# Performance work log

Hardware: AMD Instinct MI355X
Metric: run time of the kernel (lower is better)

The kernel has to match this reference:

```python
import jax, jax.numpy as jnp
import numpy as np

B, T, IN, H, OUT = 64, 32, 256, 512, 256
M, W, R = 256, 64, 4            # nr_cells, cell_size, read_heads
NN_IN = IN + R * W              # 512
NN_OUT = H + R * W              # 768
IFACE = R * W + 3 * W + 5 * R + 3  # 471
CLIP = 20.0
DELTA = 1e-6


def setup_inputs():
    key = jax.random.key(0)
    ks = jax.random.split(key, 10)
    s = 0.05
    bound = float(np.sqrt(6.0 / (B * H + 2 * H)))  # xavier_uniform on (2,B,H)
    return {
        'x': jax.random.normal(ks[0], (B, T, IN), jnp.float32),
        'h0': jax.random.uniform(ks[1], (2, B, H), jnp.float32, -bound, bound),
        'Wih0': jax.random.normal(ks[2], (4 * H, NN_IN), jnp.float32) * s,
        'Whh0': jax.random.normal(ks[3], (4 * H, H), jnp.float32) * s,
        'bih0': jnp.zeros((4 * H,), jnp.float32),
        'bhh0': jnp.zeros((4 * H,), jnp.float32),
        'Wih1': jax.random.normal(ks[4], (4 * H, H), jnp.float32) * s,
        'Whh1': jax.random.normal(ks[5], (4 * H, H), jnp.float32) * s,
        'bih1': jnp.zeros((4 * H,), jnp.float32),
        'bhh1': jnp.zeros((4 * H,), jnp.float32),
        'Wif': jax.random.normal(ks[6], (IFACE, H), jnp.float32) * s,
        'bif': jnp.zeros((IFACE,), jnp.float32),
        'Wout': jax.random.normal(ks[7], (OUT, NN_OUT), jnp.float32) * s,
        'bout': jnp.zeros((OUT,), jnp.float32),
    }


def _lstm_cell(x, h, c, Wih, Whh, bih, bhh):
    g = x @ Wih.T + bih + h @ Whh.T + bhh
    i, f, gg, o = jnp.split(g, 4, axis=1)  # torch gate order i,f,g,o
    c = jax.nn.sigmoid(f) * c + jax.nn.sigmoid(i) * jnp.tanh(gg)
    h = jax.nn.sigmoid(o) * jnp.tanh(c)
    return h, c


def _content_weights(mem, keys, strengths):
    # mem: (b,M,W), keys: (b,K,W), strengths: (b,K) -> softmax over M
    mem_n = mem / (jnp.linalg.norm(mem, axis=2, keepdims=True) + DELTA)
    key_n = keys / (jnp.linalg.norm(keys, axis=2, keepdims=True) + DELTA)
    sim = jnp.einsum('bkw,bmw->bkm', key_n, mem_n)
    return jax.nn.softmax(sim * strengths[..., None], axis=2)


def _memory_step(xi, mem, link, prec, rw, ww, usage):
    b = xi.shape[0]
    o = 0
    rk = jnp.tanh(xi[:, :R * W].reshape(b, R, W)); o = R * W
    rs = jax.nn.softplus(xi[:, o:o + R]); o += R
    wk = jnp.tanh(xi[:, o:o + W]).reshape(b, 1, W); o += W
    ws = jax.nn.softplus(xi[:, o])[:, None]; o += 1
    ev = jax.nn.sigmoid(xi[:, o:o + W]); o += W
    wv = jnp.tanh(xi[:, o:o + W]); o += W
    fg = jax.nn.sigmoid(xi[:, o:o + R]); o += R
    ag = jax.nn.sigmoid(xi[:, o])[:, None]; o += 1
    wg = jax.nn.sigmoid(xi[:, o])[:, None]; o += 1
    rm = jax.nn.softmax(xi[:, o:o + 3 * R].reshape(b, R, 3), axis=2)

    # usage update (uses OLD read/write weights); single write head
    usage = usage + (1.0 - usage) * ww
    psi = jnp.prod(1.0 - fg[:, :, None] * rw, axis=1)
    usage = usage * psi

    # write content addressing on OLD memory
    wcw = _content_weights(mem, wk, ws)[:, 0]  # (b,M)

    # allocation by ascending sort of usage (exclusive cumprod)
    u = DELTA + (1.0 - DELTA) * usage
    phi = jnp.argsort(u, axis=1)
    sorted_u = jnp.take_along_axis(u, phi, axis=1)
    excl = jnp.cumprod(jnp.concatenate([jnp.ones((b, 1), u.dtype), sorted_u], axis=1), axis=1)[:, :-1]
    sorted_alloc = (1.0 - sorted_u) * excl
    alloc = jnp.take_along_axis(sorted_alloc, jnp.argsort(phi, axis=1), axis=1)

    ww = wg * (ag * alloc + (1.0 - ag) * wcw)  # (b,M)

    # erase + write
    mem = mem * (1.0 - ww[:, :, None] * ev[:, None, :]) + ww[:, :, None] * wv[:, None, :]

    # temporal link matrix + precedence
    prev_scale = 1.0 - ww[:, :, None] - ww[:, None, :]
    link = prev_scale * link + ww[:, :, None] * prec[:, None, :]
    link = link * (1.0 - jnp.eye(M, dtype=link.dtype))
    prec = (1.0 - ww.sum(axis=1, keepdims=True)) * prec + ww

    # read: directional weights use NEW link and OLD read weights; content uses NEW memory
    rcw = _content_weights(mem, rk, rs)               # (b,R,M)
    fwd = jnp.einsum('bij,brj->bri', link, rw)
    bwd = jnp.einsum('brj,bji->bri', rw, link)
    rw = rm[:, :, 0:1] * bwd + rm[:, :, 1:2] * fwd + rm[:, :, 2:3] * rcw
    rvec = jnp.einsum('brm,bmw->brw', rw, mem).reshape(b, R * W)
    return rvec, mem, link, prec, rw, ww, usage


def reference(x, h0, Wih0, Whh0, bih0, bhh0, Wih1, Whh1, bih1, bhh1, Wif, bif, Wout, bout):
    b = x.shape[0]
    lr0 = jnp.zeros((b, R * W), x.dtype)  # initial last_read; NOTE: source concatenates this
    # initial zero last_read to EVERY timestep's controller input (inputs built upfront)
    carry0 = (h0[0], h0[0], h0[1], h0[1],
              jnp.full((b, M, W), DELTA, x.dtype),   # memory
              jnp.zeros((b, M, M), x.dtype),          # link matrix
              jnp.zeros((b, M), x.dtype),             # precedence
              jnp.full((b, R, M), DELTA, x.dtype),    # read weights
              jnp.full((b, M), DELTA, x.dtype),       # write weights
              jnp.zeros((b, M), x.dtype))             # usage

    def step(carry, x_t):
        h0_, c0_, h1_, c1_, mem, link, prec, rw, ww, usage = carry
        inp = jnp.concatenate([x_t, lr0], axis=1)
        h0_, c0_ = _lstm_cell(inp, h0_, c0_, Wih0, Whh0, bih0, bhh0)
        h1_, c1_ = _lstm_cell(h0_, h1_, c1_, Wih1, Whh1, bih1, bhh1)
        out = jnp.clip(h1_, -CLIP, CLIP)
        xi = out @ Wif.T + bif
        rvec, mem, link, prec, rw, ww, usage = _memory_step(xi, mem, link, prec, rw, ww, usage)
        o_t = jnp.concatenate([out, rvec], axis=1)  # (b, NN_OUT)
        return (h0_, c0_, h1_, c1_, mem, link, prec, rw, ww, usage), o_t

    _, ys = jax.lax.scan(step, carry0, jnp.swapaxes(x, 0, 1))  # (T,b,NN_OUT)
    outputs = jnp.tanh(ys) @ Wout.T + bout  # Dropout(p=0) -> Tanh -> Linear
    return jnp.swapaxes(outputs, 0, 1)      # (b,T,OUT)
```

## Files before the change

kernel.cpp:

```cpp
#include <hip/hip_runtime.h>
#include <hip/hip_bf16.h>
#include <math.h>


typedef __bf16 bf16_t;
typedef __attribute__((ext_vector_type(8))) __bf16 bf16x8;
typedef __attribute__((ext_vector_type(4))) float f32x4;

#define B_    64
#define T_    32
#define IN_   256
#define H_    512
#define M_    256
#define W_    64
#define R_    4
#define IFACE_ 471
#define DELTA_ 1e-6f

#define OFF_H0SEQ  (0L)
#define SZ_H0SEQ   (32L*64*512*2)
#define OFF_OUTSEQ (OFF_H0SEQ + SZ_H0SEQ)
#define SZ_OUTSEQ  (32L*64*512*2)
#define OFF_H0BUF  (OFF_OUTSEQ + SZ_OUTSEQ)
#define SZ_HBUF    (2L*64*512*2)
#define OFF_H1BUF  (OFF_H0BUF + SZ_HBUF)
#define OFF_XI     (OFF_H1BUF + SZ_HBUF)
#define SZ_XI      (32L*64*480*4)
#define OFF_RVEC   (OFF_XI + SZ_XI)
#define SZ_RVEC    (32L*64*256*4)
#define OFF_YBF    (OFF_RVEC + SZ_RVEC)
#define SZ_YBF     (32L*64*768*2)
#define OFF_BAR    (OFF_YBF + SZ_YBF)
#define SZ_BAR     (256L)
#define OFF_XB     (OFF_BAR + SZ_BAR)
#define SZ_XB      (64L*32*256*2)
#define OFF_H0B    (OFF_XB + SZ_XB)
#define SZ_H0B     (2L*64*512*2)
#define OFF_W0     (OFF_H0B + SZ_H0B)
#define SZ_W       (2048L*512*2)
#define OFF_W1     (OFF_W0 + SZ_W)
#define OFF_W2     (OFF_W1 + SZ_W)
#define OFF_W3     (OFF_W2 + SZ_W)
#define OFF_WIF    (OFF_W3 + SZ_W)
#define SZ_WIF     (480L*512*2)
#define OFF_WOUTB  (OFF_WIF + SZ_WIF)
#define SZ_WOUTB   (256L*768*2)
#define OFF_BS0    (OFF_WOUTB + SZ_WOUTB)
#define SZ_BS      (2048L*4)
#define OFF_BS1    (OFF_BS0 + SZ_BS)
#define OFF_BIF    (OFF_BS1 + SZ_BS)
#define SZ_BIF     (2048L)
#define OFF_BOUTF  (OFF_BIF + SZ_BIF)
#define SZ_BOUTF   (1024L)
#define OFF_FLG    (OFF_BOUTF + SZ_BOUTF)
#define SZ_FLG     (4096L)

__device__ __forceinline__ float frcp(float x){ return __builtin_amdgcn_rcpf(x); }
__device__ __forceinline__ float fsqrt_(float x){ return __builtin_amdgcn_sqrtf(x); }
__device__ __forceinline__ float sigf(float x){ return frcp(1.0f + __expf(-x)); }
__device__ __forceinline__ float tanh_f(float x){
  float xc = fminf(fmaxf(x, -44.0f), 44.0f);
  float t = __expf(2.0f * xc);
  return (t - 1.0f) * frcp(t + 1.0f);
}
__device__ __forceinline__ float softplusf(float x){
  return fmaxf(x, 0.0f) + __logf(1.0f + __expf(-fabsf(x)));
}
__device__ __forceinline__ float wred(float v){
  #pragma unroll
  for (int off = 32; off; off >>= 1) v += __shfl_xor(v, off, 64);
  return v;
}
__device__ __forceinline__ float ldin(const void* p, long i, int mf){
  return mf ? ((const float*)p)[i] : (float)((const bf16_t*)p)[i];
}

__device__ __forceinline__ unsigned flag_ld(const unsigned* p){
  return __hip_atomic_load(p, __ATOMIC_RELAXED, __HIP_MEMORY_SCOPE_AGENT);
}

__device__ __forceinline__ void flagbar(unsigned* flg, int bid, unsigned tgt,
                                        int tid, int lane, int wv){
  __syncthreads();
  if (tid == 0)
    __hip_atomic_store(flg + (size_t)bid*16, tgt, __ATOMIC_RELEASE,
                       __HIP_MEMORY_SCOPE_AGENT);
  if (wv == 0){
    for (;;){
      unsigned f = flag_ld(flg + (size_t)lane*16);
      if (__all(f >= tgt)) break;
      __builtin_amdgcn_s_sleep(2);
    }
    __builtin_amdgcn_fence(__ATOMIC_ACQUIRE, "agent");
  }
  __syncthreads();
}

__global__ void k_detect(const unsigned short* __restrict__ x16,
                         int* __restrict__ flag, unsigned* __restrict__ bar,
                         unsigned* __restrict__ flg){
  __shared__ int cnt;
  if (threadIdx.x == 0){ cnt = 0; bar[0] = 0u; bar[1] = 0u; }
  for (int i = threadIdx.x; i < 1024; i += 256) flg[i] = 0u;
  __syncthreads();
  unsigned short u = x16[threadIdx.x * 2];
  int e = (u >> 7) & 0xFF;
  if (e >= 0x88) atomicAdd(&cnt, 1);
  __syncthreads();
  if (threadIdx.x == 0) *flag = (cnt > 16) ? 1 : 0;
}

__global__ void k_convert(const void* x, const void* h0, const void* Wih0,
                          const void* Whh0, const void* bih0, const void* bhh0,
                          const void* Wih1, const void* Whh1, const void* bih1,
                          const void* bhh1, const void* Wif, const void* bif,
                          const void* Wout, const void* bout,
                          bf16_t* __restrict__ xb, bf16_t* __restrict__ h0b,
                          bf16_t* __restrict__ h0buf, bf16_t* __restrict__ h1buf,
                          bf16_t* __restrict__ W0, bf16_t* __restrict__ W1,
                          bf16_t* __restrict__ W2, bf16_t* __restrict__ W3,
                          bf16_t* __restrict__ Wifp, bf16_t* __restrict__ Woutb,
                          float* __restrict__ bs0, float* __restrict__ bs1,
                          float* __restrict__ bifp, float* __restrict__ boutf,
                          const int* __restrict__ flag)
{
  const int mf = *flag;
  const long stride = (long)gridDim.x * blockDim.x;
  long i0 = (long)blockIdx.x * blockDim.x + threadIdx.x;
  switch (blockIdx.y){
  case 0: for (long i = i0; i < 64L*32*256; i += stride) xb[i] = (bf16_t)ldin(x, i, mf); break;
  case 1: for (long i = i0; i < 2L*64*512; i += stride){
            float v = ldin(h0, i, mf); bf16_t bb = (bf16_t)v; h0b[i] = bb;
            if (i < 64*512) h0buf[i] = bb; else h1buf[i - 64*512] = bb;
          } break;
  case 2: for (long i = i0; i < 2048L*512; i += stride) W0[i] = (bf16_t)ldin(Wih0, i, mf); break;
  case 3: for (long i = i0; i < 2048L*512; i += stride) W1[i] = (bf16_t)ldin(Whh0, i, mf); break;
  case 4: for (long i = i0; i < 2048L*512; i += stride) W2[i] = (bf16_t)ldin(Wih1, i, mf); break;
  case 5: for (long i = i0; i < 2048L*512; i += stride) W3[i] = (bf16_t)ldin(Whh1, i, mf); break;
  case 6: for (long i = i0; i < 480L*512; i += stride){
            long r = i >> 9;
            Wifp[i] = (r < IFACE_) ? (bf16_t)ldin(Wif, i, mf) : (bf16_t)0.0f;
          } break;
  case 7: for (long i = i0; i < 256L*768; i += stride) Woutb[i] = (bf16_t)ldin(Wout, i, mf); break;
  case 8:
    for (long i = i0; i < 2048; i += stride){
      bs0[i] = ldin(bih0, i, mf) + ldin(bhh0, i, mf);
      bs1[i] = ldin(bih1, i, mf) + ldin(bhh1, i, mf);
    }
    for (long i = i0; i < 480; i += stride) bifp[i] = (i < IFACE_) ? ldin(bif, i, mf) : 0.0f;
    for (long i = i0; i < 256; i += stride) boutf[i] = ldin(bout, i, mf);
    break;
  }
}

__device__ __forceinline__ void softmax256_wave(float* a, int lane){
  float v0=a[lane], v1=a[64+lane], v2=a[128+lane], v3=a[192+lane];
  float mx = fmaxf(fmaxf(v0,v1), fmaxf(v2,v3));
  #pragma unroll
  for (int off=32; off; off>>=1) mx = fmaxf(mx, __shfl_xor(mx, off, 64));
  v0=__expf(v0-mx); v1=__expf(v1-mx); v2=__expf(v2-mx); v3=__expf(v3-mx);
  float s = v0+v1+v2+v3;
  #pragma unroll
  for (int off=32; off; off>>=1) s += __shfl_xor(s, off, 64);
  float inv = frcp(s);
  a[lane]=v0*inv; a[64+lane]=v1*inv; a[128+lane]=v2*inv; a[192+lane]=v3*inv;
}

struct ProdShm {
  bf16_t wpool[66560];
  float  cst[64][16];
  float  bias[4][16];
};
struct ConsShm {
  float smem[256][65];
  float rkn4r[2][65][4];
  float wkn[64], ev_[64], wvv[64];
  float rs_[4], fg_[4], rm_[4][3];
  float wsS, agS, wgS, wwsumS;
  float invn[256], wcw[256];
  float usage[256], uu[256], su[256], scanA[256];
  int   rank_[256];
  float ww_[256], prec_[256];
  float rw_[4][256];
  float rw4[256][4];
  float fwd_[4][256], bwd_[4][256], rcw_[4][256];
  bf16_t rwb[4][264];
  float p2cT[2][264];
  float p5cT[5][2][264];
};
union ShUnion { ProdShm p; ConsShm c; };

__global__ __launch_bounds__(512) void k_main(
    const bf16_t* __restrict__ xb, const bf16_t* __restrict__ h0b,
    const bf16_t* __restrict__ W0, const bf16_t* __restrict__ W1,
    const bf16_t* __restrict__ W2, const bf16_t* __restrict__ W3,
    const float* __restrict__ bs0, const float* __restrict__ bs1,
    const bf16_t* __restrict__ Wifp, const float* __restrict__ bifp,
    bf16_t* __restrict__ h0buf, bf16_t* __restrict__ h1buf,
    bf16_t* __restrict__ h0seq, bf16_t* __restrict__ outseq,
    float* __restrict__ XI, float* __restrict__ RVEC,
    unsigned* __restrict__ flg)
{
  __shared__ ShUnion sh;
  const int bid = blockIdx.x;
  const int tid = threadIdx.x, lane = tid & 63, wv = tid >> 6;
  const int m16 = lane & 15, q = lane >> 4;

  if (bid < 64){
    ProdShm& P = sh.p;
    const int layer = bid >> 5;
    const int u0 = (bid & 31) * 16;

    if (!layer){
      for (int i = tid; i < 64*32; i += 512){
        int rl = i >> 5, c8 = (i & 31)*8;
        int grow = (rl >> 4)*512 + u0 + (rl & 15);
        *(bf16x8*)&P.wpool[rl*264 + c8] = *(const bf16x8*)(W0 + (size_t)grow*512 + c8);
      }
      for (int i = tid; i < 64*64; i += 512){
        int rl = i >> 6, c8 = (i & 63)*8;
        int grow = (rl >> 4)*512 + u0 + (rl & 15);
        *(bf16x8*)&P.wpool[16896 + rl*520 + c8] = *(const bf16x8*)(W1 + (size_t)grow*512 + c8);
      }
    } else {
      for (int i = tid; i < 64*64; i += 512){
        int rl = i >> 6, c8 = (i & 63)*8;
        int grow = (rl >> 4)*512 + u0 + (rl & 15);
        *(bf16x8*)&P.wpool[rl*520 + c8]         = *(const bf16x8*)(W2 + (size_t)grow*512 + c8);
        *(bf16x8*)&P.wpool[33280 + rl*520 + c8] = *(const bf16x8*)(W3 + (size_t)grow*512 + c8);
      }
    }
    for (int i = tid; i < 64*16; i += 512){
      int b = i >> 4, n = i & 15;
      P.cst[b][n] = (float)h0b[layer*(64*512) + b*512 + u0 + n];
    }
    if (tid < 64){
      int G = tid >> 4, n = tid & 15;
      const float* bs = layer ? bs1 : bs0;
      P.bias[G][n] = bs[G*512 + u0 + n];
    }
    __syncthreads();

    bf16_t* hbuf = layer ? h1buf : h0buf;

    for (int ps = 0; ps <= 33; ++ps){
      if (wv < 4){
        const int t = layer ? (ps - 1) : ps;
        const bool active = layer ? (ps >= 1 && ps <= 32) : (ps < 32);
        if (active){
          const int p = t & 1;
          const bf16_t* hin = hbuf + p*(64*512);
          bf16_t* hout = hbuf + (p^1)*(64*512);
          const int b0 = wv * 16;

          f32x4 acc[4];
          #pragma unroll
          for (int G = 0; G < 4; ++G){ float bv = P.bias[G][m16]; acc[G] = (f32x4){bv,bv,bv,bv}; }

          if (!layer){
            #pragma unroll 2
            for (int kt = 0; kt < 8; ++kt){
              bf16x8 a = *(const bf16x8*)(xb + ((size_t)(b0+m16)*T_ + t)*IN_ + kt*32 + q*8);
              #pragma unroll
              for (int G = 0; G < 4; ++G)
                acc[G] = __builtin_amdgcn_mfma_f32_16x16x32_bf16(
                    a, *(const bf16x8*)&P.wpool[(G*16+m16)*264 + kt*32 + q*8], acc[G], 0, 0, 0);
            }
            #pragma unroll 4
            for (int kt = 0; kt < 16; ++kt){
              bf16x8 a = *(const bf16x8*)(hin + (b0+m16)*512 + kt*32 + q*8);
              #pragma unroll
              for (int G = 0; G < 4; ++G)
                acc[G] = __builtin_amdgcn_mfma_f32_16x16x32_bf16(
                    a, *(const bf16x8*)&P.wpool[16896 + (G*16+m16)*520 + kt*32 + q*8], acc[G], 0, 0, 0);
            }
          } else {
            #pragma unroll 4
            for (int kt = 0; kt < 16; ++kt){
              bf16x8 a = *(const bf16x8*)(h0seq + ((size_t)t*64 + b0+m16)*512 + kt*32 + q*8);
              #pragma unroll
              for (int G = 0; G < 4; ++G)
                acc[G] = __builtin_amdgcn_mfma_f32_16x16x32_bf16(
                    a, *(const bf16x8*)&P.wpool[(G*16+m16)*520 + kt*32 + q*8], acc[G], 0, 0, 0);
            }
            #pragma unroll 4
            for (int kt = 0; kt < 16; ++kt){
              bf16x8 a = *(const bf16x8*)(hin + (b0+m16)*512 + kt*32 + q*8);
              #pragma unroll
              for (int G = 0; G < 4; ++G)
                acc[G] = __builtin_amdgcn_mfma_f32_16x16x32_bf16(
                    a, *(const bf16x8*)&P.wpool[33280 + (G*16+m16)*520 + kt*32 + q*8], acc[G], 0, 0, 0);
            }
          }
          #pragma unroll
          for (int v = 0; v < 4; ++v){
            int b = b0 + q*4 + v;
            float gi = acc[0][v], gf = acc[1][v], gg = acc[2][v], go = acc[3][v];
            float c_ = sigf(gf)*P.cst[b][m16] + sigf(gi)*tanh_f(gg);
            P.cst[b][m16] = c_;
            float h = sigf(go)*tanh_f(c_);
            bf16_t hb = (bf16_t)h;
            hout[b*512 + u0 + m16] = hb;
            if (!layer) h0seq[((size_t)t*64 + b)*512 + u0 + m16] = hb;
            else        outseq[((size_t)t*64 + b)*512 + u0 + m16] = hb;
          }
        }
      } else if (ps >= 2 && bid < 30){
        const int t2 = ps - 2;
        const int b0 = (wv - 4) * 16;
        const int r = bid*16 + m16;
        float bv = bifp[r];
        f32x4 acc = {bv,bv,bv,bv};
        const bf16_t* arow = outseq + ((size_t)t2*64 + b0 + m16)*512 + q*8;
        const bf16_t* brow = Wifp + (size_t)r*512 + q*8;
        #pragma unroll 4
        for (int kt = 0; kt < 16; ++kt){
          acc = __builtin_amdgcn_mfma_f32_16x16x32_bf16(
              *(const bf16x8*)(arow + kt*32), *(const bf16x8*)(brow + kt*32), acc, 0, 0, 0);
        }
        #pragma unroll
        for (int v = 0; v < 4; ++v)
          XI[((size_t)t2*64 + b0 + q*4 + v)*480 + r] = acc[v];
      }
      flagbar(flg, bid, (unsigned)(ps + 1), tid, lane, wv);
    }
  } else {
    ConsShm& S = sh.c;
    const int b = bid - 64;
    const int quad = lane >> 4, li = lane & 15;

    bf16x8 rowL[2][8], colL[2][8];
    #pragma unroll
    for (int g = 0; g < 2; ++g)
      #pragma unroll
      for (int ch = 0; ch < 8; ++ch)
        #pragma unroll
        for (int z = 0; z < 8; ++z){ rowL[g][ch][z] = (bf16_t)0.0f; colL[g][ch][z] = (bf16_t)0.0f; }

    float mr[32];
    #pragma unroll
    for (int z = 0; z < 32; ++z) mr[z] = DELTA_;

    int off0 = -1, off1 = -1, off2 = -1;
    if (wv < 4)            off0 = wv*64 + lane;
    else if (wv == 4)      off0 = 260 + lane;
    else if (wv == 5)      off0 = 325 + lane;
    else if (wv == 6)      off0 = 389 + lane;
    else {
      if (lane < 4)        off0 = 256 + lane;
      else if (lane == 4)  off0 = 324;
      else if (lane < 9)   off0 = 453 + (lane - 5);
      else if (lane == 9)  off0 = 457;
      else if (lane == 10) off0 = 458;
      else if (lane >= 16 && lane < 20){
        off0 = 459 + (lane - 16)*3; off1 = off0 + 1; off2 = off0 + 2;
      }
    }

    if (tid < 256){
      S.ww_[tid] = DELTA_; S.usage[tid] = 0.0f; S.prec_[tid] = 0.0f;
      S.invn[tid] = 1.0f/(fsqrt_(64.0f*DELTA_*DELTA_) + DELTA_);
      #pragma unroll
      for (int r = 0; r < 4; ++r) S.rw_[r][tid] = DELTA_;
    }
    for (int i = tid; i < 4*264; i += 512) ((bf16_t*)S.rwb)[i] = (bf16_t)DELTA_;
    for (int i = tid; i < 256*65; i += 512) ((float*)S.smem)[i] = DELTA_;
    __syncthreads();

    const int mH = tid >> 1, q2 = tid & 1;

    if (wv == 0){
      for (;;){
        unsigned f = flag_ld(flg + (size_t)lane*16);
        if (__all(f >= 3u)) break;
        __builtin_amdgcn_s_sleep(2);
      }
      __builtin_amdgcn_fence(__ATOMIC_ACQUIRE, "agent");
    }
    __syncthreads();
    float x0 = 0.0f, x1 = 0.0f, x2 = 0.0f;
    {
      const float* xp = XI + (size_t)b*480;
      if (off0 >= 0) x0 = xp[off0];
      if (off1 >= 0){ x1 = xp[off1]; x2 = xp[off2]; }
    }

    for (int t = 0; t < 32; ++t){
      if (wv < 4){
        float v = tanh_f(x0);
        float s = wred(v*v);
        float vn = v * frcp(fsqrt_(s) + DELTA_);
        S.rkn4r[0][lane][wv] = vn; S.rkn4r[1][lane][wv] = vn;
      } else if (wv == 4){
        float v = tanh_f(x0);
        float s = wred(v*v);
        S.wkn[lane] = v * frcp(fsqrt_(s) + DELTA_);
      } else if (wv == 5){ S.ev_[lane] = sigf(x0);
      } else if (wv == 6){ S.wvv[lane] = tanh_f(x0);
      } else {
        if (lane < 4)        S.rs_[lane] = softplusf(x0);
        else if (lane == 4)  S.wsS = softplusf(x0);
        else if (lane < 9)   S.fg_[lane-5] = sigf(x0);
        else if (lane == 9)  S.agS = sigf(x0);
        else if (lane == 10) S.wgS = sigf(x0);
        else if (lane >= 16 && lane < 20){
          int r = lane - 16;
          float mx = fmaxf(x0, fmaxf(x1, x2));
          float e0 = __expf(x0-mx), e1 = __expf(x1-mx), e2 = __expf(x2-mx);
          float inv = frcp(e0+e1+e2);
          S.rm_[r][0]=e0*inv; S.rm_[r][1]=e1*inv; S.rm_[r][2]=e2*inv;
        }
      }
      __syncthreads();

      if (tid < 256){
        int m = tid;
        float us = S.usage[m] + (1.0f - S.usage[m])*S.ww_[m];
        float psi = (1.0f - S.fg_[0]*S.rw_[0][m]) * (1.0f - S.fg_[1]*S.rw_[1][m])
                  * (1.0f - S.fg_[2]*S.rw_[2][m]) * (1.0f - S.fg_[3]*S.rw_[3][m]);
        us *= psi;
        S.usage[m] = us;
        S.uu[m] = DELTA_ + (1.0f - DELTA_)*us;
      }
      { float acc = 0.0f;
        #pragma unroll
        for (int it = 0; it < 32; ++it){
          int w = q2*32 + it;
          acc += mr[it] * S.wkn[w];
        }
        S.p2cT[q2][mH] = acc; }
      __syncthreads();

      if (wv == 0){
        #pragma unroll
        for (int z = 0; z < 4; ++z){
          int m = z*64 + lane;
          S.wcw[m] = S.wsS * (S.p2cT[0][m] + S.p2cT[1][m]) * S.invn[m];
        }
        softmax256_wave(S.wcw, lane);
      } else if (tid >= 256){
        const int i = tid - 256;
        const float ui = S.uu[i];
        int cnt = 0;
        #pragma unroll 8
        for (int k = 0; k < 64; ++k){
          f32x4 u4 = *(const f32x4*)&S.uu[k*4];
          #pragma unroll
          for (int z = 0; z < 4; ++z){
            int j = k*4 + z; float uj = u4[z];
            cnt += (uj < ui || (uj == ui && j < i)) ? 1 : 0;
          }
        }
        S.rank_[i] = cnt;
        S.su[cnt] = ui;
      }
      __syncthreads();

      if (wv == 0){
        int base = lane*4;
        float v0 = S.su[base], v1 = S.su[base+1], v2 = S.su[base+2];
        float p1 = v0*v1, p2 = p1*v2, p3 = p2*S.su[base+3];
        float sc = p3;
        #pragma unroll
        for (int off = 1; off < 64; off <<= 1){
          float n = __shfl_up(sc, off, 64);
          if (lane >= off) sc *= n;
        }
        float exch = __shfl_up(sc, 1, 64);
        if (lane == 0) exch = 1.0f;
        S.scanA[base] = exch; S.scanA[base+1] = exch*v0;
        S.scanA[base+2] = exch*p1; S.scanA[base+3] = exch*p2;
      }
      __syncthreads();

      { const int m = mH;
        float al = (1.0f - S.uu[m]) * S.scanA[S.rank_[m]];
        float wm = S.wgS*(S.agS*al + (1.0f - S.agS)*S.wcw[m]);
        if (q2 == 0) S.ww_[m] = wm;
        float s2 = 0.0f, sr0 = 0.0f, sr1 = 0.0f, sr2 = 0.0f, sr3 = 0.0f;
        #pragma unroll
        for (int it = 0; it < 32; ++it){
          int w = q2*32 + it;
          float mn = mr[it]*(1.0f - wm*S.ev_[w]) + wm*S.wvv[w];
          mr[it] = mn;
          S.smem[m][w] = mn;
          s2 += mn*mn;
          f32x4 rk = *(const f32x4*)&S.rkn4r[q2][w][0];
          sr0 += mn*rk[0]; sr1 += mn*rk[1]; sr2 += mn*rk[2]; sr3 += mn*rk[3];
        }
        S.p5cT[0][q2][m] = s2;
        S.p5cT[1][q2][m] = sr0; S.p5cT[2][q2][m] = sr1;
        S.p5cT[3][q2][m] = sr2; S.p5cT[4][q2][m] = sr3; }
      __syncthreads();

      if (tid < 256){
        int m = tid;
        float s2 = S.p5cT[0][0][m] + S.p5cT[0][1][m];
        float inv = frcp(fsqrt_(s2) + DELTA_);
        S.invn[m] = inv;
        #pragma unroll
        for (int r = 0; r < 4; ++r){
          float sr = S.p5cT[r+1][0][m] + S.p5cT[r+1][1][m];
          S.rcw_[r][m] = S.rs_[r]*sr*inv;
        }
      } else if (wv == 4){
        float s = wred(S.ww_[lane] + S.ww_[64+lane] + S.ww_[128+lane] + S.ww_[192+lane]);
        if (lane == 0) S.wwsumS = s;
      }
      { float wown[2], pown[2], alpha[2];
        #pragma unroll
        for (int g = 0; g < 2; ++g){
          int o = wv*32 + g*16 + li;
          wown[g] = S.ww_[o]; pown[g] = S.prec_[o];
          alpha[g] = 1.0f - wown[g];
        }
        f32x4 facc[2] = {{0,0,0,0},{0,0,0,0}}, bacc[2] = {{0,0,0,0},{0,0,0,0}};
        #pragma unroll
        for (int ch = 0; ch < 8; ++ch){
          const int cbase = ch*32 + quad*8;
          bf16x8 rwf = *(const bf16x8*)&S.rwb[li & 3][cbase];
          f32x4 wA = *(const f32x4*)&S.ww_[cbase];
          f32x4 wB = *(const f32x4*)&S.ww_[cbase+4];
          f32x4 pA = *(const f32x4*)&S.prec_[cbase];
          f32x4 pB = *(const f32x4*)&S.prec_[cbase+4];
          float wcf[8] = {wA[0],wA[1],wA[2],wA[3],wB[0],wB[1],wB[2],wB[3]};
          float pcf[8] = {pA[0],pA[1],pA[2],pA[3],pB[0],pB[1],pB[2],pB[3]};
          #pragma unroll
          for (int g = 0; g < 2; ++g){
            const int o = wv*32 + g*16 + li;
            bf16x8 rl = rowL[g][ch];
            bf16x8 cl = colL[g][ch];
            #pragma unroll
            for (int jj = 0; jj < 8; ++jj){
              const int c = cbase + jj;
              float s = alpha[g] - wcf[jj];
              float vr = s*(float)rl[jj] + wown[g]*pcf[jj];
              float vc = s*(float)cl[jj] + wcf[jj]*pown[g];
              if (c == o){ vr = 0.0f; vc = 0.0f; }
              rl[jj] = (bf16_t)vr;
              cl[jj] = (bf16_t)vc;
            }
            rowL[g][ch] = rl; colL[g][ch] = cl;
            facc[g] = __builtin_amdgcn_mfma_f32_16x16x32_bf16(rl, rwf, facc[g], 0, 0, 0);
            bacc[g] = __builtin_amdgcn_mfma_f32_16x16x32_bf16(rwf, cl, bacc[g], 0, 0, 0);
          }
        }
        #pragma unroll
        for (int g = 0; g < 2; ++g){
          if (li < 4){
            #pragma unroll
            for (int z = 0; z < 4; ++z) S.fwd_[li][wv*32 + g*16 + quad*4 + z] = facc[g][z];
          }
          if (quad == 0){
            #pragma unroll
            for (int z = 0; z < 4; ++z) S.bwd_[z][wv*32 + g*16 + li] = bacc[g][z];
          }
        }
      }
      __syncthreads();

      if (wv < 4) softmax256_wave(S.rcw_[wv], lane);
      else {
        int m = tid - 256;
        float p = (1.0f - S.wwsumS)*S.prec_[m] + S.ww_[m];
        S.prec_[m] = p;
        if (wv == 4 && t < 31){
          const unsigned tgt = (unsigned)(t + 4);
          for (;;){
            unsigned f = flag_ld(flg + (size_t)lane*16);
            if (__all(f >= tgt)) break;
            __builtin_amdgcn_s_sleep(2);
          }
          __builtin_amdgcn_fence(__ATOMIC_ACQUIRE, "agent");
        }
      }
      __syncthreads();

      if (t < 31){
        const float* xp = XI + ((size_t)(t+1)*64 + b)*480;
        if (off0 >= 0) x0 = xp[off0];
        if (off1 >= 0){ x1 = xp[off1]; x2 = xp[off2]; }
      }
      { int r = tid >> 7, m0 = (tid & 127)*2;
        #pragma unroll
        for (int z = 0; z < 2; ++z){
          int m = m0 + z;
          float v = S.rm_[r][0]*S.bwd_[r][m] + S.rm_[r][1]*S.fwd_[r][m] + S.rm_[r][2]*S.rcw_[r][m];
          S.rw_[r][m] = v;
          S.rw4[m][r] = v;
          S.rwb[r][m] = (bf16_t)v;
        } }
      __syncthreads();

      { const int o = tid >> 1;
        const int r = o >> 6, w = o & 63;
        float s = 0.0f;
        #pragma unroll 16
        for (int k = 0; k < 128; ++k){
          int m = q2*128 + k;
          s += S.rw4[m][r] * S.smem[m][w];
        }
        s += __shfl_xor(s, 1, 64);
        if (q2 == 0) RVEC[((size_t)t*64 + b)*256 + o] = s;
      }
    }
  }
}

__global__ void k_tanhy(const bf16_t* __restrict__ outseq, const float* __restrict__ RVEC,
                        bf16_t* __restrict__ Y){
  const int n = 2048*768;
  for (int i = blockIdx.x*blockDim.x + threadIdx.x; i < n; i += gridDim.x*blockDim.x){
    int row = i / 768, j = i - row*768;
    float v = (j < 512) ? (float)outseq[(size_t)row*512 + j] : RVEC[(size_t)row*256 + (j - 512)];
    Y[i] = (bf16_t)tanh_f(v);
  }
}

__global__ __launch_bounds__(256,1) void k_out(
    const bf16_t* __restrict__ Y, const bf16_t* __restrict__ Woutb,
    const float* __restrict__ boutf, void* __restrict__ dout,
    const int* __restrict__ flag)
{
  const int mf = *flag;
  const int mt = blockIdx.x;
  const int tid = threadIdx.x, lane = tid & 63, wv = tid >> 6;
  const int nt = blockIdx.y*4 + wv;
  const int m16 = lane & 15, q = lane >> 4;
  const int o = nt*16 + m16;
  float bv = boutf[o];
  f32x4 acc = {bv,bv,bv,bv};
  const bf16_t* arow = Y + (size_t)(mt*16 + m16)*768 + q*8;
  const bf16_t* brow = Woutb + (size_t)o*768 + q*8;
  for (int kt = 0; kt < 24; ++kt){
    acc = __builtin_amdgcn_mfma_f32_16x16x32_bf16(
        *(const bf16x8*)(arow + kt*32), *(const bf16x8*)(brow + kt*32), acc, 0, 0, 0);
  }
  #pragma unroll
  for (int v = 0; v < 4; ++v){
    int row = mt*16 + q*4 + v;
    int b = row & 63, t = row >> 6;
    size_t idx = ((size_t)b*T_ + t)*256 + o;
    if (mf) ((float*)dout)[idx] = acc[v];
    else    ((bf16_t*)dout)[idx] = (bf16_t)acc[v];
  }
}

extern "C" void kernel_launch(void* const* d_in, const int* in_sizes, int n_in,
                              void* d_out, int out_size, void* d_ws, size_t ws_size,
                              hipStream_t stream)
{
  char* ws = (char*)d_ws;
  bf16_t* H0SEQ  = (bf16_t*)(ws + OFF_H0SEQ);
  bf16_t* OUTSEQ = (bf16_t*)(ws + OFF_OUTSEQ);
  bf16_t* H0BUF  = (bf16_t*)(ws + OFF_H0BUF);
  bf16_t* H1BUF  = (bf16_t*)(ws + OFF_H1BUF);
  float*  XI     = (float*) (ws + OFF_XI);
  float*  RVEC   = (float*) (ws + OFF_RVEC);
  bf16_t* YBF    = (bf16_t*)(ws + OFF_YBF);
  unsigned* BAR  = (unsigned*)(ws + OFF_BAR);
  int*    FLAG   = (int*)   (ws + OFF_BAR + 8);
  bf16_t* XB     = (bf16_t*)(ws + OFF_XB);
  bf16_t* H0B    = (bf16_t*)(ws + OFF_H0B);
  bf16_t* W0     = (bf16_t*)(ws + OFF_W0);
  bf16_t* W1     = (bf16_t*)(ws + OFF_W1);
  bf16_t* W2     = (bf16_t*)(ws + OFF_W2);
  bf16_t* W3     = (bf16_t*)(ws + OFF_W3);
  bf16_t* WIFP   = (bf16_t*)(ws + OFF_WIF);
  bf16_t* WOUTB  = (bf16_t*)(ws + OFF_WOUTB);
  float*  BS0    = (float*) (ws + OFF_BS0);
  float*  BS1    = (float*) (ws + OFF_BS1);
  float*  BIFP   = (float*) (ws + OFF_BIF);
  float*  BOUTF  = (float*) (ws + OFF_BOUTF);
  unsigned* FLG  = (unsigned*)(ws + OFF_FLG);

  k_detect<<<1, 256, 0, stream>>>((const unsigned short*)d_in[0], FLAG, BAR, FLG);
  k_convert<<<dim3(256, 9), 256, 0, stream>>>(
      d_in[0], d_in[1], d_in[2], d_in[3], d_in[4], d_in[5], d_in[6],
      d_in[7], d_in[8], d_in[9], d_in[10], d_in[11], d_in[12], d_in[13],
      XB, H0B, H0BUF, H1BUF, W0, W1, W2, W3, WIFP, WOUTB,
      BS0, BS1, BIFP, BOUTF, FLAG);
  k_main<<<128, 512, 0, stream>>>(XB, H0B, W0, W1, W2, W3, BS0, BS1,
                                  WIFP, BIFP, H0BUF, H1BUF, H0SEQ, OUTSEQ,
                                  XI, RVEC, FLG);
  k_tanhy<<<512, 256, 0, stream>>>(OUTSEQ, RVEC, YBF);
  k_out<<<dim3(128, 4), 256, 0, stream>>>(YBF, WOUTB, BOUTF, d_out, FLAG);
}
```

Before: 1.099 ms.

## Double block size to 1024 threads and repartition memory-step work across waves

Launches the persistent main kernel with 1024 threads per block. Consumer blocks split their per-row memory, link-matrix and read-vector work over 16 waves instead of 8: each thread holds fewer memory columns and link rows, the usage sort rank is computed in two halves and then combined, and the read-vector product becomes per-wave partial sums followed by a reduction. The aim is to shorten the serial per-timestep latency of the memory update by adding parallelism. In exchange it adds synchronisation barriers and shared-memory traffic, and the producer blocks' extra waves sit mostly idle while register pressure per thread is capped.

```diff
diff --git a/kernel.cpp b/kernel.cpp
--- a/kernel.cpp
+++ b/kernel.cpp
@@ -173,24 +173,26 @@
 };
 struct ConsShm {
   float smem[256][65];
-  float rkn4r[2][65][4];
+  float rkn4r[4][65][4];
   float wkn[64], ev_[64], wvv[64];
   float rs_[4], fg_[4], rm_[4][3];
   float wsS, agS, wgS, wwsumS;
   float invn[256], wcw[256];
   float usage[256], uu[256], su[256], scanA[256];
   int   rank_[256];
+  int   rankP[2][256];
   float ww_[256], prec_[256];
   float rw_[4][256];
   float rw4[256][4];
   float fwd_[4][256], bwd_[4][256], rcw_[4][256];
   bf16_t rwb[4][264];
-  float p2cT[2][264];
-  float p5cT[5][2][264];
+  float p4cT[4][264];
+  float p5cT[5][4][264];
+  float rvp[16][4][64];
 };
 union ShUnion { ProdShm p; ConsShm c; };
 
-__global__ __launch_bounds__(512) void k_main(
+__global__ __launch_bounds__(1024) void k_main(
     const bf16_t* __restrict__ xb, const bf16_t* __restrict__ h0b,
     const bf16_t* __restrict__ W0, const bf16_t* __restrict__ W1,
     const bf16_t* __restrict__ W2, const bf16_t* __restrict__ W3,
@@ -212,25 +214,25 @@
     const int u0 = (bid & 31) * 16;
 
     if (!layer){
-      for (int i = tid; i < 64*32; i += 512){
+      for (int i = tid; i < 64*32; i += 1024){
         int rl = i >> 5, c8 = (i & 31)*8;
         int grow = (rl >> 4)*512 + u0 + (rl & 15);
         *(bf16x8*)&P.wpool[rl*264 + c8] = *(const bf16x8*)(W0 + (size_t)grow*512 + c8);
       }
-      for (int i = tid; i < 64*64; i += 512){
+      for (int i = tid; i < 64*64; i += 1024){
         int rl = i >> 6, c8 = (i & 63)*8;
         int grow = (rl >> 4)*512 + u0 + (rl & 15);
         *(bf16x8*)&P.wpool[16896 + rl*520 + c8] = *(const bf16x8*)(W1 + (size_t)grow*512 + c8);
       }
     } else {
-      for (int i = tid; i < 64*64; i += 512){
+      for (int i = tid; i < 64*64; i += 1024){
         int rl = i >> 6, c8 = (i & 63)*8;
         int grow = (rl >> 4)*512 + u0 + (rl & 15);
         *(bf16x8*)&P.wpool[rl*520 + c8]         = *(const bf16x8*)(W2 + (size_t)grow*512 + c8);
         *(bf16x8*)&P.wpool[33280 + rl*520 + c8] = *(const bf16x8*)(W3 + (size_t)grow*512 + c8);
       }
     }
-    for (int i = tid; i < 64*16; i += 512){
+    for (int i = tid; i < 64*16; i += 1024){
       int b = i >> 4, n = i & 15;
       P.cst[b][n] = (float)h0b[layer*(64*512) + b*512 + u0 + n];
     }
@@ -305,7 +307,7 @@
             else        outseq[((size_t)t*64 + b)*512 + u0 + m16] = hb;
           }
         }
-      } else if (ps >= 2 && bid < 30){
+      } else if (wv < 8 && ps >= 2 && bid < 30){
         const int t2 = ps - 2;
         const int b0 = (wv - 4) * 16;
         const int r = bid*16 + m16;
@@ -329,24 +331,24 @@
     const int b = bid - 64;
     const int quad = lane >> 4, li = lane & 15;
 
-    bf16x8 rowL[2][8], colL[2][8];
+    const int orow = wv*16 + li;
+    bf16x8 rowL[8], colL[8];
     #pragma unroll
-    for (int g = 0; g < 2; ++g)
+    for (int ch = 0; ch < 8; ++ch)
       #pragma unroll
-      for (int ch = 0; ch < 8; ++ch)
-        #pragma unroll
-        for (int z = 0; z < 8; ++z){ rowL[g][ch][z] = (bf16_t)0.0f; colL[g][ch][z] = (bf16_t)0.0f; }
-
-    float mr[32];
+      for (int z = 0; z < 8; ++z){ rowL[ch][z] = (bf16_t)0.0f; colL[ch][z] = (bf16_t)0.0f; }
+
+    const int mQ = tid >> 2, q4 = tid & 3;
+    float mr[16];
     #pragma unroll
-    for (int z = 0; z < 32; ++z) mr[z] = DELTA_;
+    for (int z = 0; z < 16; ++z) mr[z] = DELTA_;
 
     int off0 = -1, off1 = -1, off2 = -1;
     if (wv < 4)            off0 = wv*64 + lane;
     else if (wv == 4)      off0 = 260 + lane;
     else if (wv == 5)      off0 = 325 + lane;
     else if (wv == 6)      off0 = 389 + lane;
-    else {
+    else if (wv == 7){
       if (lane < 4)        off0 = 256 + lane;
       else if (lane == 4)  off0 = 324;
       else if (lane < 9)   off0 = 453 + (lane - 5);
@@ -363,11 +365,9 @@
       #pragma unroll
       for (int r = 0; r < 4; ++r) S.rw_[r][tid] = DELTA_;
     }
-    for (int i = tid; i < 4*264; i += 512) ((bf16_t*)S.rwb)[i] = (bf16_t)DELTA_;
-    for (int i = tid; i < 256*65; i += 512) ((float*)S.smem)[i] = DELTA_;
+    for (int i = tid; i < 4*264; i += 1024) ((bf16_t*)S.rwb)[i] = (bf16_t)DELTA_;
+    for (int i = tid; i < 256*65; i += 1024) ((float*)S.smem)[i] = DELTA_;
     __syncthreads();
-
-    const int mH = tid >> 1, q2 = tid & 1;
 
     if (wv == 0){
       for (;;){
@@ -390,14 +390,15 @@
         float v = tanh_f(x0);
         float s = wred(v*v);
         float vn = v * frcp(fsqrt_(s) + DELTA_);
-        S.rkn4r[0][lane][wv] = vn; S.rkn4r[1][lane][wv] = vn;
+        #pragma unroll
+        for (int g = 0; g < 4; ++g) S.rkn4r[g][lane][wv] = vn;
       } else if (wv == 4){
         float v = tanh_f(x0);
         float s = wred(v*v);
         S.wkn[lane] = v * frcp(fsqrt_(s) + DELTA_);
       } else if (wv == 5){ S.ev_[lane] = sigf(x0);
       } else if (wv == 6){ S.wvv[lane] = tanh_f(x0);
-      } else {
+      } else if (wv == 7){
         if (lane < 4)        S.rs_[lane] = softplusf(x0);
         else if (lane == 4)  S.wsS = softplusf(x0);
         else if (lane < 9)   S.fg_[lane-5] = sigf(x0);
@@ -424,35 +425,42 @@
       }
       { float acc = 0.0f;
         #pragma unroll
-        for (int it = 0; it < 32; ++it){
-          int w = q2*32 + it;
+        for (int it = 0; it < 16; ++it){
+          int w = q4*16 + it;
           acc += mr[it] * S.wkn[w];
         }
-        S.p2cT[q2][mH] = acc; }
+        S.p4cT[q4][mQ] = acc; }
       __syncthreads();
 
       if (wv == 0){
         #pragma unroll
         for (int z = 0; z < 4; ++z){
           int m = z*64 + lane;
-          S.wcw[m] = S.wsS * (S.p2cT[0][m] + S.p2cT[1][m]) * S.invn[m];
+          S.wcw[m] = S.wsS * (S.p4cT[0][m] + S.p4cT[1][m] + S.p4cT[2][m] + S.p4cT[3][m]) * S.invn[m];
         }
         softmax256_wave(S.wcw, lane);
-      } else if (tid >= 256){
-        const int i = tid - 256;
+      } else if (tid >= 512){
+        const int idx = tid - 512;
+        const int i = idx & 255, half = idx >> 8;
         const float ui = S.uu[i];
         int cnt = 0;
         #pragma unroll 8
-        for (int k = 0; k < 64; ++k){
-          f32x4 u4 = *(const f32x4*)&S.uu[k*4];
+        for (int k = 0; k < 32; ++k){
+          f32x4 u4 = *(const f32x4*)&S.uu[half*128 + k*4];
           #pragma unroll
           for (int z = 0; z < 4; ++z){
-            int j = k*4 + z; float uj = u4[z];
+            int j = half*128 + k*4 + z; float uj = u4[z];
             cnt += (uj < ui || (uj == ui && j < i)) ? 1 : 0;
           }
         }
-        S.rank_[i] = cnt;
-        S.su[cnt] = ui;
+        S.rankP[half][i] = cnt;
+      }
+      __syncthreads();
+
+      if (tid < 256){
+        int rank = S.rankP[0][tid] + S.rankP[1][tid];
+        S.rank_[tid] = rank;
+        S.su[rank] = S.uu[tid];
       }
       __syncthreads();
 
@@ -473,48 +481,42 @@
       }
       __syncthreads();
 
-      { const int m = mH;
-        float al = (1.0f - S.uu[m]) * S.scanA[S.rank_[m]];
-        float wm = S.wgS*(S.agS*al + (1.0f - S.agS)*S.wcw[m]);
-        if (q2 == 0) S.ww_[m] = wm;
+      { float al = (1.0f - S.uu[mQ]) * S.scanA[S.rank_[mQ]];
+        float wm = S.wgS*(S.agS*al + (1.0f - S.agS)*S.wcw[mQ]);
+        if (q4 == 0) S.ww_[mQ] = wm;
         float s2 = 0.0f, sr0 = 0.0f, sr1 = 0.0f, sr2 = 0.0f, sr3 = 0.0f;
         #pragma unroll
-        for (int it = 0; it < 32; ++it){
-          int w = q2*32 + it;
+        for (int it = 0; it < 16; ++it){
+          int w = q4*16 + it;
           float mn = mr[it]*(1.0f - wm*S.ev_[w]) + wm*S.wvv[w];
           mr[it] = mn;
-          S.smem[m][w] = mn;
+          S.smem[mQ][w] = mn;
           s2 += mn*mn;
-          f32x4 rk = *(const f32x4*)&S.rkn4r[q2][w][0];
+          f32x4 rk = *(const f32x4*)&S.rkn4r[q4][w][0];
           sr0 += mn*rk[0]; sr1 += mn*rk[1]; sr2 += mn*rk[2]; sr3 += mn*rk[3];
         }
-        S.p5cT[0][q2][m] = s2;
-        S.p5cT[1][q2][m] = sr0; S.p5cT[2][q2][m] = sr1;
-        S.p5cT[3][q2][m] = sr2; S.p5cT[4][q2][m] = sr3; }
+        S.p5cT[0][q4][mQ] = s2;
+        S.p5cT[1][q4][mQ] = sr0; S.p5cT[2][q4][mQ] = sr1;
+        S.p5cT[3][q4][mQ] = sr2; S.p5cT[4][q4][mQ] = sr3; }
       __syncthreads();
 
       if (tid < 256){
         int m = tid;
-        float s2 = S.p5cT[0][0][m] + S.p5cT[0][1][m];
+        float s2 = S.p5cT[0][0][m] + S.p5cT[0][1][m] + S.p5cT[0][2][m] + S.p5cT[0][3][m];
         float inv = frcp(fsqrt_(s2) + DELTA_);
         S.invn[m] = inv;
         #pragma unroll
         for (int r = 0; r < 4; ++r){
-          float sr = S.p5cT[r+1][0][m] + S.p5cT[r+1][1][m];
+          float sr = S.p5cT[r+1][0][m] + S.p5cT[r+1][1][m] + S.p5cT[r+1][2][m] + S.p5cT[r+1][3][m];
           S.rcw_[r][m] = S.rs_[r]*sr*inv;
         }
       } else if (wv == 4){
         float s = wred(S.ww_[lane] + S.ww_[64+lane] + S.ww_[128+lane] + S.ww_[192+lane]);
         if (lane == 0) S.wwsumS = s;
       }
-      { float wown[2], pown[2], alpha[2];
-        #pragma unroll
-        for (int g = 0; g < 2; ++g){
-          int o = wv*32 + g*16 + li;
-          wown[g] = S.ww_[o]; pown[g] = S.prec_[o];
-          alpha[g] = 1.0f - wown[g];
-        }
-        f32x4 facc[2] = {{0,0,0,0},{0,0,0,0}}, bacc[2] = {{0,0,0,0},{0,0,0,0}};
+      { const float wown = S.ww_[orow], pown = S.prec_[orow];
+        const float alpha = 1.0f - wown;
+        f32x4 facc = {0,0,0,0}, bacc = {0,0,0,0};
         #pragma unroll
         for (int ch = 0; ch < 8; ++ch){
           const int cbase = ch*32 + quad*8;
@@ -525,83 +527,80 @@
           f32x4 pB = *(const f32x4*)&S.prec_[cbase+4];
           float wcf[8] = {wA[0],wA[1],wA[2],wA[3],wB[0],wB[1],wB[2],wB[3]};
           float pcf[8] = {pA[0],pA[1],pA[2],pA[3],pB[0],pB[1],pB[2],pB[3]};
+          bf16x8 rl = rowL[ch];
+          bf16x8 cl = colL[ch];
           #pragma unroll
-          for (int g = 0; g < 2; ++g){
-            const int o = wv*32 + g*16 + li;
-            bf16x8 rl = rowL[g][ch];
-            bf16x8 cl = colL[g][ch];
-            #pragma unroll
-            for (int jj = 0; jj < 8; ++jj){
-              const int c = cbase + jj;
-              float s = alpha[g] - wcf[jj];
-              float vr = s*(float)rl[jj] + wown[g]*pcf[jj];
-              float vc = s*(float)cl[jj] + wcf[jj]*pown[g];
-              if (c == o){ vr = 0.0f; vc = 0.0f; }
-              rl[jj] = (bf16_t)vr;
-              cl[jj] = (bf16_t)vc;
-            }
-            rowL[g][ch] = rl; colL[g][ch] = cl;
-            facc[g] = __builtin_amdgcn_mfma_f32_16x16x32_bf16(rl, rwf, facc[g], 0, 0, 0);
-            bacc[g] = __builtin_amdgcn_mfma_f32_16x16x32_bf16(rwf, cl, bacc[g], 0, 0, 0);
+          for (int jj = 0; jj < 8; ++jj){
+            const int c = cbase + jj;
+            float s = alpha - wcf[jj];
+            float vr = s*(float)rl[jj] + wown*pcf[jj];
+            float vc = s*(float)cl[jj] + wcf[jj]*pown;
+            if (c == orow){ vr = 0.0f; vc = 0.0f; }
+            rl[jj] = (bf16_t)vr;
+            cl[jj] = (bf16_t)vc;
           }
-        }
-        #pragma unroll
-        for (int g = 0; g < 2; ++g){
-          if (li < 4){
-            #pragma unroll
-            for (int z = 0; z < 4; ++z) S.fwd_[li][wv*32 + g*16 + quad*4 + z] = facc[g][z];
-          }
-          if (quad == 0){
-            #pragma unroll
-            for (int z = 0; z < 4; ++z) S.bwd_[z][wv*32 + g*16 + li] = bacc[g][z];
-          }
+          rowL[ch] = rl; colL[ch] = cl;
+          facc = __builtin_amdgcn_mfma_f32_16x16x32_bf16(rl, rwf, facc, 0, 0, 0);
+          bacc = __builtin_amdgcn_mfma_f32_16x16x32_bf16(rwf, cl, bacc, 0, 0, 0);
+        }
+        if (li < 4){
+          #pragma unroll
+          for (int z = 0; z < 4; ++z) S.fwd_[li][wv*16 + quad*4 + z] = facc[z];
+        }
+        if (quad == 0){
+          #pragma unroll
+          for (int z = 0; z < 4; ++z) S.bwd_[z][wv*16 + li] = bacc[z];
         }
       }
       __syncthreads();
 
       if (wv < 4) softmax256_wave(S.rcw_[wv], lane);
-      else {
-        int m = tid - 256;
+      else if (tid >= 512 && tid < 768){
+        int m = tid - 512;
         float p = (1.0f - S.wwsumS)*S.prec_[m] + S.ww_[m];
         S.prec_[m] = p;
-        if (wv == 4 && t < 31){
-          const unsigned tgt = (unsigned)(t + 4);
-          for (;;){
-            unsigned f = flag_ld(flg + (size_t)lane*16);
-            if (__all(f >= tgt)) break;
-            __builtin_amdgcn_s_sleep(2);
-          }
-          __builtin_amdgcn_fence(__ATOMIC_ACQUIRE, "agent");
-        }
-      }
-      __syncthreads();
-
-      if (t < 31){
+      } else if (wv == 15 && t < 31){
+        const unsigned tgt = (unsigned)(t + 4);
+        for (;;){
+          unsigned f = flag_ld(flg + (size_t)lane*16);
+          if (__all(f >= tgt)) break;
+          __builtin_amdgcn_s_sleep(2);
+        }
+        __builtin_amdgcn_fence(__ATOMIC_ACQUIRE, "agent");
+      }
+      __syncthreads();
+
+      if (t < 31 && off0 >= 0){
         const float* xp = XI + ((size_t)(t+1)*64 + b)*480;
-        if (off0 >= 0) x0 = xp[off0];
+        x0 = xp[off0];
         if (off1 >= 0){ x1 = xp[off1]; x2 = xp[off2]; }
       }
-      { int r = tid >> 7, m0 = (tid & 127)*2;
-        #pragma unroll
-        for (int z = 0; z < 2; ++z){
-          int m = m0 + z;
-          float v = S.rm_[r][0]*S.bwd_[r][m] + S.rm_[r][1]*S.fwd_[r][m] + S.rm_[r][2]*S.rcw_[r][m];
-          S.rw_[r][m] = v;
-          S.rw4[m][r] = v;
-          S.rwb[r][m] = (bf16_t)v;
-        } }
-      __syncthreads();
-
-      { const int o = tid >> 1;
-        const int r = o >> 6, w = o & 63;
-        float s = 0.0f;
-        #pragma unroll 16
-        for (int k = 0; k < 128; ++k){
-          int m = q2*128 + k;
-          s += S.rw4[m][r] * S.smem[m][w];
-        }
-        s += __shfl_xor(s, 1, 64);
-        if (q2 == 0) RVEC[((size_t)t*64 + b)*256 + o] = s;
+      { const int r = tid >> 8, m = tid & 255;
+        float v = S.rm_[r][0]*S.bwd_[r][m] + S.rm_[r][1]*S.fwd_[r][m] + S.rm_[r][2]*S.rcw_[r][m];
+        S.rw_[r][m] = v;
+        S.rw4[m][r] = v;
+        S.rwb[r][m] = (bf16_t)v;
+      }
+      __syncthreads();
+
+      { float r0 = 0, r1 = 0, r2 = 0, r3 = 0;
+        #pragma unroll
+        for (int k = 0; k < 16; ++k){
+          int m = wv*16 + k;
+          f32x4 r4 = *(const f32x4*)&S.rw4[m][0];
+          float mv = S.smem[m][lane];
+          r0 += r4[0]*mv; r1 += r4[1]*mv; r2 += r4[2]*mv; r3 += r4[3]*mv;
+        }
+        S.rvp[wv][0][lane] = r0; S.rvp[wv][1][lane] = r1;
+        S.rvp[wv][2][lane] = r2; S.rvp[wv][3][lane] = r3; }
+      __syncthreads();
+
+      if (tid < 256){
+        const int w = tid & 63, r = tid >> 6;
+        float v = 0.0f;
+        #pragma unroll
+        for (int c = 0; c < 16; ++c) v += S.rvp[c][r][w];
+        RVEC[((size_t)t*64 + b)*256 + tid] = v;
       }
     }
   }
@@ -680,9 +679,9 @@
       d_in[7], d_in[8], d_in[9], d_in[10], d_in[11], d_in[12], d_in[13],
       XB, H0B, H0BUF, H1BUF, W0, W1, W2, W3, WIFP, WOUTB,
       BS0, BS1, BIFP, BOUTF, FLAG);
-  k_main<<<128, 512, 0, stream>>>(XB, H0B, W0, W1, W2, W3, BS0, BS1,
-                                  WIFP, BIFP, H0BUF, H1BUF, H0SEQ, OUTSEQ,
-                                  XI, RVEC, FLG);
+  k_main<<<128, 1024, 0, stream>>>(XB, H0B, W0, W1, W2, W3, BS0, BS1,
+                                   WIFP, BIFP, H0BUF, H1BUF, H0SEQ, OUTSEQ,
+                                   XI, RVEC, FLG);
   k_tanhy<<<512, 256, 0, stream>>>(OUTSEQ, RVEC, YBF);
   k_out<<<dim3(128, 4), 256, 0, stream>>>(YBF, WOUTB, BOUTF, d_out, FLAG);
 }
```

Result: faster. 1.014 ms (-7.7%).
